# Optimization experiments

Measured on AMD Instinct MI355X. Metric: run time of the kernel, lower is better.

## Reference

```python
import jax, jax.numpy as jnp
import numpy as np

SEQ, B, IN_DIM, HID, OUT_DIM = 1024, 256, 131, 256, 131


def setup_inputs() -> dict:
    key = jax.random.key(0)
    ks = jax.random.split(key, 24)
    def p(k, shape):
        return (jax.random.normal(k, shape, dtype=jnp.float32) * 0.1)
    inp = {
        'X': jax.random.normal(ks[0], (SEQ, B, IN_DIM), dtype=jnp.float32),
        'Y': jax.random.normal(ks[1], (SEQ - 1, B, IN_DIM), dtype=jnp.float32),
        # encoder layer 0 (input -> hidden) and layer 1 (hidden -> hidden)
        'enc_Wih0': p(ks[2], (HID, IN_DIM)), 'enc_Whh0': p(ks[3], (HID, HID)),
        'enc_bih0': p(ks[4], (HID,)),        'enc_bhh0': p(ks[5], (HID,)),
        'enc_Wih1': p(ks[6], (HID, HID)),    'enc_Whh1': p(ks[7], (HID, HID)),
        'enc_bih1': p(ks[8], (HID,)),        'enc_bhh1': p(ks[9], (HID,)),
        # decoder RNNCells
        'dec_Wih0': p(ks[10], (HID, IN_DIM)), 'dec_Whh0': p(ks[11], (HID, HID)),
        'dec_bih0': p(ks[12], (HID,)),        'dec_bhh0': p(ks[13], (HID,)),
        'dec_Wih1': p(ks[14], (HID, HID)),    'dec_Whh1': p(ks[15], (HID, HID)),
        'dec_bih1': p(ks[16], (HID,)),        'dec_bhh1': p(ks[17], (HID,)),
        # output projection
        'lin_W': p(ks[18], (OUT_DIM, HID)), 'lin_b': p(ks[19], (OUT_DIM,)),
    }
    return inp


def _rnn_layer(seq, h0, Wih, Whh, bih, bhh):
    # Elman RNN layer: h_t = tanh(x_t Wih^T + bih + h_{t-1} Whh^T + bhh)
    def step(h, x):
        h = jnp.tanh(x @ Wih.T + bih + h @ Whh.T + bhh)
        return h, h
    hT, outs = jax.lax.scan(step, h0, seq)
    return outs, hT


def reference(X, Y,
              enc_Wih0, enc_Whh0, enc_bih0, enc_bhh0,
              enc_Wih1, enc_Whh1, enc_bih1, enc_bhh1,
              dec_Wih0, dec_Whh0, dec_bih0, dec_bhh0,
              dec_Wih1, dec_Whh1, dec_bih1, dec_bhh1,
              lin_W, lin_b):
    B_ = X.shape[1]
    H = enc_Whh0.shape[0]
    h0 = jnp.zeros((B_, H), X.dtype)
    # Encoder consumes X[:-1]
    out0, hn0 = _rnn_layer(X[:-1], h0, enc_Wih0, enc_Whh0, enc_bih0, enc_bhh0)
    out1, hn1 = _rnn_layer(out0, h0, enc_Wih1, enc_Whh1, enc_bih1, enc_bhh1)
    # Decoder (teacher forcing): inputs are X[-1], Y[0], ..., Y[T_out-2]
    T_out = X.shape[0] - 1
    dec_in = jnp.concatenate([X[-1:], Y[:T_out - 1]], axis=0)  # [T_out, B, in_dim]
    def dec_step(carry, x):
        h0c, h1c = carry
        h0n = jnp.tanh(x @ dec_Wih0.T + dec_bih0 + h0c @ dec_Whh0.T + dec_bhh0)
        h1n = jnp.tanh(h0n @ dec_Wih1.T + dec_bih1 + h1c @ dec_Whh1.T + dec_bhh1)
        logits = h1n @ lin_W.T + lin_b
        return (h0n, h1n), jax.nn.log_softmax(logits, axis=-1)
    _, Ypred = jax.lax.scan(dec_step, (hn0, hn1), dec_in)
    return Ypred  # [T_out, B, out_dim]
```

## Files before the change

### kernel.cpp

```cpp
#include <hip/hip_runtime.h>
#include <cstddef>


typedef __attribute__((ext_vector_type(8))) short short8;
typedef __attribute__((ext_vector_type(4))) float f32x4;

namespace {
constexpr int TSTEPS = 1023;
constexpr int BATCH = 256;
constexpr int IND = 131;
constexpr int OUTD = 131;
constexpr int MTOT = TSTEPS * BATCH;

constexpr size_t SB = (size_t)MTOT * 256 * 4;
constexpr int UE0 = 0;
constexpr int UE1 = 131072;
constexpr int UD0 = 262144;
constexpr int UD1 = 393216;
constexpr int EW0 = 524288;
constexpr int DW0 = 606208;
constexpr int EW1 = 688128;
constexpr int DW1 = 819200;
constexpr int LINP = 950272;
constexpr int PK_USH = 1024000;
constexpr size_t PKB = 2 * SB;
constexpr size_t BFB = PKB + 2 * (size_t)PK_USH;
constexpr int FIN0 = 1168;
constexpr int FIN1 = 1168 + 65536;
constexpr size_t TOTAL_WS = BFB + (size_t)(1168 + 2 * 65536) * 4;

constexpr int OFF_EW0s = 0, OFF_EH0s = 33792, OFF_EW1s = 99328, OFF_EH1s = 164864;
constexpr int OFF_DW0s = 230400, OFF_DH0s = 264192, OFF_DW1s = 329728, OFF_DH1s = 395264;
constexpr int OFF_LWs = 460800, OFF_EB0s = 494336, OFF_EB1s = 494592;
constexpr int OFF_DB0s = 494848, OFF_DB1s = 495104;
constexpr int WS_TOTAL_SLOW = 495360;
}

__device__ __forceinline__ unsigned short f2bf(float x) {
  unsigned u = __float_as_uint(x);
  u += 0x7fffu + ((u >> 16) & 1u);
  return (unsigned short)(u >> 16);
}
__device__ __forceinline__ float bf2f(unsigned short h) {
  return __uint_as_float(((unsigned)h) << 16);
}
__device__ __forceinline__ float ftanh(float x) {
  const float ax = fabsf(x);
  const float e = __expf(-2.f * ax);
  const float t = __fdividef(1.f - e, 1.f + e);
  return copysignf(t, x);
}
__device__ __forceinline__ f32x4 mfma16(uint4 a, uint4 b, f32x4 c) {
  return __builtin_amdgcn_mfma_f32_16x16x32_bf16(
      __builtin_bit_cast(short8, a), __builtin_bit_cast(short8, b), c, 0, 0, 0);
}

__global__ void prep_pack(
    const float* __restrict__ eW0, const float* __restrict__ eH0,
    const float* __restrict__ eb_ih0, const float* __restrict__ eb_hh0,
    const float* __restrict__ eW1, const float* __restrict__ eH1,
    const float* __restrict__ eb_ih1, const float* __restrict__ eb_hh1,
    const float* __restrict__ dW0, const float* __restrict__ dH0,
    const float* __restrict__ db_ih0, const float* __restrict__ db_hh0,
    const float* __restrict__ dW1, const float* __restrict__ dH1,
    const float* __restrict__ db_ih1, const float* __restrict__ db_hh1,
    const float* __restrict__ linW, const float* __restrict__ linb,
    unsigned short* __restrict__ pk, float* __restrict__ bfin) {
  const int e = blockIdx.x * 256 + threadIdx.x;
  if (e >= 513168) return;
  if (e < 262144) {
    const int um = e >> 16, le = e & 65535;
    const int j = le & 7, lane = (le >> 3) & 63, tile = (le >> 9) & 15, kk = le >> 13;
    const int n = tile * 16 + (lane & 15), k = kk * 32 + ((lane >> 4) << 3) + j;
    const float* U = (um == 0) ? eH0 : (um == 1) ? eH1 : (um == 2) ? dH0 : dH1;
    const float x = U[n * 256 + k];
    const unsigned short h = f2bf(x);
    const int base = um * 131072;
    pk[base + le] = h;
    pk[base + 65536 + le] = f2bf(x - bf2f(h));
  } else if (e < 344064) {
    const bool isD = (e >= 303104);
    const int e2 = e - (isD ? 303104 : 262144);
    const int j = e2 & 7, lane = (e2 >> 3) & 63, tile = (e2 >> 9) & 15, kk = e2 >> 13;
    const int n = tile * 16 + (lane & 15), k = kk * 32 + ((lane >> 4) << 3) + j;
    const float* W = isD ? dW0 : eW0;
    const float x = (k < IND) ? W[n * IND + k] : 0.f;
    const unsigned short h = f2bf(x);
    const int base = isD ? DW0 : EW0;
    pk[base + e2] = h;
    pk[base + 40960 + e2] = f2bf(x - bf2f(h));
  } else if (e < 475136) {
    const bool isD = (e >= 409600);
    const int e2 = e - (isD ? 409600 : 344064);
    const int j = e2 & 7, lane = (e2 >> 3) & 63, tile = (e2 >> 9) & 15, kk = e2 >> 13;
    const int n = tile * 16 + (lane & 15), k = kk * 32 + ((lane >> 4) << 3) + j;
    const float* W = isD ? dW1 : eW1;
    const float x = W[n * 256 + k];
    const unsigned short h = f2bf(x);
    const int base = isD ? DW1 : EW1;
    pk[base + e2] = h;
    pk[base + 65536 + e2] = f2bf(x - bf2f(h));
  } else if (e < 512000) {
    const int e2 = e - 475136;
    const int kk = e2 / 4608;
    const int rem = e2 - kk * 4608;
    const int t9 = rem >> 9, le = rem & 511;
    const int j = le & 7, lane = le >> 3;
    const int n = t9 * 16 + (lane & 15), k = kk * 32 + ((lane >> 4) << 3) + j;
    const float x = (n < OUTD) ? linW[n * 256 + k] : 0.f;
    const unsigned short h = f2bf(x);
    pk[LINP + e2] = h;
    pk[LINP + 36864 + e2] = f2bf(x - bf2f(h));
  } else {
    const int e3 = e - 512000;
    if (e3 < 256) bfin[e3] = eb_ih0[e3] + eb_hh0[e3];
    else if (e3 < 512) { const int j = e3 - 256; bfin[e3] = eb_ih1[j] + eb_hh1[j]; }
    else if (e3 < 768) { const int j = e3 - 512; bfin[e3] = db_ih0[j] + db_hh0[j]; }
    else if (e3 < 1024){ const int j = e3 - 768; bfin[e3] = db_ih1[j] + db_hh1[j]; }
    else { const int j = e3 - 1024; bfin[e3] = (j < OUTD) ? linb[j] : -1e30f; }
  }
}

__global__ __launch_bounds__(256) void gemm_proj(
    const float* __restrict__ A, const float* __restrict__ X1023,
    const float* __restrict__ Yp, const int amode, const int K, const int KK,
    const unsigned short* __restrict__ Wh, const unsigned short* __restrict__ Wl,
    const float* __restrict__ bias, float* __restrict__ Pout) {
  __shared__ unsigned short Ah[64][40];
  __shared__ unsigned short Al[64][40];
  const int tid = threadIdx.x, lane = tid & 63, wid = tid >> 6;
  const int mbase = blockIdx.x * 64;
  const int cg = blockIdx.y;
  const int srow = tid >> 2, kidx = (tid & 3) << 3;
  const float* rowptr;
  {
    const int grow = mbase + srow;
    if (amode) {
      const int t = grow >> 8, b = grow & 255;
      rowptr = t ? (Yp + ((size_t)(t - 1) * 256 + b) * IND) : (X1023 + (size_t)b * IND);
    } else {
      rowptr = A + (size_t)grow * K;
    }
  }
  const f32x4 z = {0.f, 0.f, 0.f, 0.f};
  f32x4 acc[4] = {z, z, z, z};
  const uint4* Wh4 = (const uint4*)Wh;
  const uint4* Wl4 = (const uint4*)Wl;
  for (int kk = 0; kk < KK; ++kk) {
    const int k0 = kk << 5;
    __syncthreads();
    float v[8];
#pragma unroll
    for (int j = 0; j < 8; ++j) {
      const int kg = k0 + kidx + j;
      v[j] = (kg < K) ? rowptr[kg] : 0.f;
    }
#pragma unroll
    for (int j = 0; j < 8; ++j) {
      const unsigned short h = f2bf(v[j]);
      Ah[srow][kidx + j] = h;
      Al[srow][kidx + j] = f2bf(v[j] - bf2f(h));
    }
    __syncthreads();
    const uint4 avh = *(const uint4*)&Ah[(wid << 4) + (lane & 15)][(lane >> 4) << 3];
    const uint4 avl = *(const uint4*)&Al[(wid << 4) + (lane & 15)][(lane >> 4) << 3];
#pragma unroll
    for (int tt = 0; tt < 4; ++tt) {
      const int bi = ((kk << 4) + (cg << 2) + tt) * 64 + lane;
      const uint4 bh = Wh4[bi], bl = Wl4[bi];
      acc[tt] = mfma16(avh, bh, acc[tt]);
      acc[tt] = mfma16(avh, bl, acc[tt]);
      acc[tt] = mfma16(avl, bh, acc[tt]);
    }
  }
#pragma unroll
  for (int tt = 0; tt < 4; ++tt) {
    const int col = ((cg << 2) + tt) * 16 + (lane & 15);
    const float bcol = bias[col];
#pragma unroll
    for (int r = 0; r < 4; ++r) {
      const int row = mbase + (wid << 4) + ((lane >> 4) << 2) + r;
      Pout[(size_t)row * 256 + col] = acc[tt][r] + bcol;
    }
  }
}

__global__ __launch_bounds__(512, 2) void scan_kernel(
    const float* __restrict__ Pin, float* __restrict__ Pout,
    const unsigned short* __restrict__ Uh,
    const float* __restrict__ hinit, float* __restrict__ finals) {
  __shared__ unsigned short Ah[2][16][264];
  __shared__ unsigned short Al[2][16][264];
  const int tid = threadIdx.x, lane = tid & 63, wid = tid >> 6;
  const int r0 = blockIdx.x << 4;
  const uint4* U4 = (const uint4*)Uh;
  uint4 uf[2][2][8];
#pragma unroll
  for (int tt = 0; tt < 2; ++tt)
#pragma unroll
    for (int kk = 0; kk < 8; ++kk) {
      const int idx = ((kk << 4) + wid * 2 + tt) * 64 + lane;
      uf[0][tt][kk] = U4[idx];
      uf[1][tt][kk] = U4[idx + 8192];
    }
#pragma unroll
  for (int j = 0; j < 8; ++j) {
    const int e = tid * 8 + j;
    const int row = e >> 8, col = e & 255;
    const float x = hinit ? hinit[((r0 + row) << 8) + col] : 0.f;
    const unsigned short h = f2bf(x);
    Ah[0][row][col] = h;
    Al[0][row][col] = f2bf(x - bf2f(h));
  }
  __syncthreads();
  const int rowl = (lane >> 4) << 2;
  const int col0 = (wid * 2) * 16 + (lane & 15);
  const float* pin_base = Pin + (((size_t)(r0 + rowl)) << 8) + col0;
  float* pout_base = Pout ? (Pout + (((size_t)(r0 + rowl)) << 8) + col0) : (float*)0;
  float* fbase = finals ? (finals + (((size_t)(r0 + rowl)) << 8) + col0) : (float*)0;
  float pc[2][4];
#pragma unroll
  for (int tt = 0; tt < 2; ++tt)
#pragma unroll
    for (int r = 0; r < 4; ++r) pc[tt][r] = pin_base[tt * 16 + r * 256];
  for (int t = 0; t < TSTEPS; ++t) {
    const int cur = t & 1, nxt = cur ^ 1;
    float pn[2][4];
    {
      const int tn = (t + 1 < TSTEPS) ? (t + 1) : t;
      const float* ptn = pin_base + (size_t)tn * 65536;
#pragma unroll
      for (int tt = 0; tt < 2; ++tt)
#pragma unroll
        for (int r = 0; r < 4; ++r) pn[tt][r] = ptn[tt * 16 + r * 256];
    }
    const f32x4 z = {0.f, 0.f, 0.f, 0.f};
    f32x4 hh[2] = {z, z}, hl[2] = {z, z}, lh[2] = {z, z};
#pragma unroll
    for (int kk = 0; kk < 8; ++kk) {
      const uint4 avh = *(const uint4*)&Ah[cur][lane & 15][(kk << 5) + ((lane >> 4) << 3)];
      const uint4 avl = *(const uint4*)&Al[cur][lane & 15][(kk << 5) + ((lane >> 4) << 3)];
      hh[0] = mfma16(avh, uf[0][0][kk], hh[0]);
      hh[1] = mfma16(avh, uf[0][1][kk], hh[1]);
      hl[0] = mfma16(avh, uf[1][0][kk], hl[0]);
      hl[1] = mfma16(avh, uf[1][1][kk], hl[1]);
      lh[0] = mfma16(avl, uf[0][0][kk], lh[0]);
      lh[1] = mfma16(avl, uf[0][1][kk], lh[1]);
    }
    float* pot = pout_base ? (pout_base + (size_t)t * 65536) : (float*)0;
#pragma unroll
    for (int tt = 0; tt < 2; ++tt) {
#pragma unroll
      for (int r = 0; r < 4; ++r) {
        const float av = (hh[tt][r] + hl[tt][r]) + lh[tt][r];
        const float x = ftanh(av + pc[tt][r]);
        if (pot) pot[tt * 16 + r * 256] = x;
        if (fbase && t == TSTEPS - 1) fbase[tt * 16 + r * 256] = x;
        const unsigned short h = f2bf(x);
        Ah[nxt][rowl + r][col0 + tt * 16] = h;
        Al[nxt][rowl + r][col0 + tt * 16] = f2bf(x - bf2f(h));
      }
    }
    asm volatile("s_waitcnt lgkmcnt(0)\n\ts_barrier" ::: "memory");
#pragma unroll
    for (int tt = 0; tt < 2; ++tt)
#pragma unroll
      for (int r = 0; r < 4; ++r) pc[tt][r] = pn[tt][r];
  }
}

__global__ __launch_bounds__(256) void head_kernel(
    const float* __restrict__ A, const unsigned short* __restrict__ Wh,
    const unsigned short* __restrict__ Wl, const float* __restrict__ biasp,
    float* __restrict__ out) {
  __shared__ unsigned short Ah[64][40];
  __shared__ unsigned short Al[64][40];
  const int tid = threadIdx.x, lane = tid & 63, wid = tid >> 6;
  const int mbase = blockIdx.x * 64;
  const int srow = tid >> 2, kidx = (tid & 3) << 3;
  const float* rowptr = A + (size_t)(mbase + srow) * 256;
  const f32x4 z = {0.f, 0.f, 0.f, 0.f};
  f32x4 acc[9] = {z, z, z, z, z, z, z, z, z};
  const uint4* Wh4 = (const uint4*)Wh;
  const uint4* Wl4 = (const uint4*)Wl;
  for (int kk = 0; kk < 8; ++kk) {
    const int k0 = kk << 5;
    __syncthreads();
#pragma unroll
    for (int j = 0; j < 8; ++j) {
      const float v = rowptr[k0 + kidx + j];
      const unsigned short h = f2bf(v);
      Ah[srow][kidx + j] = h;
      Al[srow][kidx + j] = f2bf(v - bf2f(h));
    }
    __syncthreads();
    const uint4 avh = *(const uint4*)&Ah[(wid << 4) + (lane & 15)][(lane >> 4) << 3];
    const uint4 avl = *(const uint4*)&Al[(wid << 4) + (lane & 15)][(lane >> 4) << 3];
#pragma unroll
    for (int tt = 0; tt < 9; ++tt) {
      const int bi = (kk * 9 + tt) * 64 + lane;
      const uint4 bh = Wh4[bi], bl = Wl4[bi];
      acc[tt] = mfma16(avh, bh, acc[tt]);
      acc[tt] = mfma16(avh, bl, acc[tt]);
      acc[tt] = mfma16(avl, bh, acc[tt]);
    }
  }
#pragma unroll
  for (int tt = 0; tt < 9; ++tt) {
    const float b = biasp[tt * 16 + (lane & 15)];
#pragma unroll
    for (int r = 0; r < 4; ++r) acc[tt][r] += b;
  }
  float lse[4];
#pragma unroll
  for (int r = 0; r < 4; ++r) {
    float m = acc[0][r];
#pragma unroll
    for (int tt = 1; tt < 9; ++tt) m = fmaxf(m, acc[tt][r]);
    m = fmaxf(m, __shfl_xor(m, 1));
    m = fmaxf(m, __shfl_xor(m, 2));
    m = fmaxf(m, __shfl_xor(m, 4));
    m = fmaxf(m, __shfl_xor(m, 8));
    float s = 0.f;
#pragma unroll
    for (int tt = 0; tt < 9; ++tt) s += __expf(acc[tt][r] - m);
    s += __shfl_xor(s, 1);
    s += __shfl_xor(s, 2);
    s += __shfl_xor(s, 4);
    s += __shfl_xor(s, 8);
    lse[r] = m + __logf(s);
  }
#pragma unroll
  for (int tt = 0; tt < 9; ++tt) {
    const int col = tt * 16 + (lane & 15);
    if (col < OUTD) {
#pragma unroll
      for (int r = 0; r < 4; ++r) {
        const int row = mbase + (wid << 4) + ((lane >> 4) << 2) + r;
        out[(size_t)row * OUTD + col] = acc[tt][r] - lse[r];
      }
    }
  }
}

__device__ __forceinline__ void packWs(float* __restrict__ ws, const float* __restrict__ src,
                                       int e, int off, int K, int ncols) {
  const int le = e - off;
  const int m = le & 3;
  const int tt = le >> 2;
  const int j = tt % ncols;
// ... 122 lines not shown
    __syncthreads();
    h1s[0][tid] = n1a; h1s[1][tid] = n1b;
    __syncthreads();
  }
  for (int t = 0; t < TSTEPS; ++t) {
    const float* xbase = (t == 0) ? (X + (size_t)TSTEPS * BATCH * IND)
                                  : (Y + (size_t)(t - 1) * BATCH * IND);
    {
      const int r = tid / 132, i = tid - r * 132;
      xb[r][i] = (i < IND) ? xbase[(size_t)(r0 + r) * IND + i] : 0.f;
      if (tid < 8) {
        const int i2 = tid + 124;
        xb[1][i2] = (i2 < IND) ? xbase[(size_t)(r0 + 1) * IND + i2] : 0.f;
      }
    }
    __syncthreads();
    const float2 a = layer_in(dw0, dh0, xb[0], xb[1], h0s[0], h0s[1], db0v, tid);
    const float n0a = ftanh(a.x), n0b = ftanh(a.y);
    __syncthreads();
    h0s[0][tid] = n0a; h0s[1][tid] = n0b;
    __syncthreads();
    const float2 b = layer_hh(dw1, dh1, h0s[0], h0s[1], h1s[0], h1s[1], db1v, tid);
    const float n1a = ftanh(b.x), n1b = ftanh(b.y);
    __syncthreads();
    h1s[0][tid] = n1a; h1s[1][tid] = n1b;
    __syncthreads();
    if (tid < OUTD) {
      float c0 = linb[tid], c1 = linb[tid];
#pragma unroll 4
      for (int k4 = 0; k4 < 64; ++k4) {
        const float4 w = lw[k4 * OUTD + tid];
        c0 = dot4(*(const float4*)&h1s[0][k4 * 4], w, c0);
        c1 = dot4(*(const float4*)&h1s[1][k4 * 4], w, c1);
      }
      lo[0][tid] = c0;
      lo[1][tid] = c1;
    }
    __syncthreads();
    const int wid = tid >> 6, lane = tid & 63;
    if (wid < 2) {
      float m = -3.0e38f;
      for (int o = lane; o < OUTD; o += 64) m = fmaxf(m, lo[wid][o]);
#pragma unroll
      for (int off = 32; off > 0; off >>= 1) m = fmaxf(m, __shfl_xor(m, off, 64));
      float s = 0.f;
      for (int o = lane; o < OUTD; o += 64) s += __expf(lo[wid][o] - m);
#pragma unroll
      for (int off = 32; off > 0; off >>= 1) s += __shfl_xor(s, off, 64);
      const float lse = m + __logf(s);
      float* op = out + ((size_t)t * BATCH + r0 + wid) * OUTD;
      for (int o = lane; o < OUTD; o += 64) op[o] = lo[wid][o] - lse;
    }
    __syncthreads();
  }
}

extern "C" void kernel_launch(void* const* d_in, const int* in_sizes, int n_in,
                              void* d_out, int out_size, void* d_ws, size_t ws_size,
                              hipStream_t stream) {
  const float* X      = (const float*)d_in[0];
  const float* Y      = (const float*)d_in[1];
  const float* eW0    = (const float*)d_in[2];
  const float* eH0    = (const float*)d_in[3];
  const float* eb_ih0 = (const float*)d_in[4];
  const float* eb_hh0 = (const float*)d_in[5];
  const float* eW1    = (const float*)d_in[6];
  const float* eH1    = (const float*)d_in[7];
  const float* eb_ih1 = (const float*)d_in[8];
  const float* eb_hh1 = (const float*)d_in[9];
  const float* dW0    = (const float*)d_in[10];
  const float* dH0    = (const float*)d_in[11];
  const float* db_ih0 = (const float*)d_in[12];
  const float* db_hh0 = (const float*)d_in[13];
  const float* dW1    = (const float*)d_in[14];
  const float* dH1    = (const float*)d_in[15];
  const float* db_ih1 = (const float*)d_in[16];
  const float* db_hh1 = (const float*)d_in[17];
  const float* linW   = (const float*)d_in[18];
  const float* linb   = (const float*)d_in[19];
  float* out = (float*)d_out;

  if (ws_size >= TOTAL_WS) {
    float* buf0 = (float*)d_ws;
    float* buf1 = (float*)((char*)d_ws + SB);
    unsigned short* pk = (unsigned short*)((char*)d_ws + PKB);
    float* bfin = (float*)((char*)d_ws + BFB);
    float* be0 = bfin, *be1 = bfin + 256, *bd0 = bfin + 512, *bd1 = bfin + 768;
    float* blin = bfin + 1024;
    float* fin0 = bfin + FIN0;
    float* fin1 = bfin + FIN1;
    const float* X1023 = X + (size_t)TSTEPS * BATCH * IND;

    prep_pack<<<2005, 256, 0, stream>>>(eW0, eH0, eb_ih0, eb_hh0, eW1, eH1, eb_ih1,
                                        eb_hh1, dW0, dH0, db_ih0, db_hh0, dW1, dH1,
                                        db_ih1, db_hh1, linW, linb, pk, bfin);
    gemm_proj<<<dim3(MTOT / 64, 4), 256, 0, stream>>>(
        X, nullptr, nullptr, 0, IND, 5, pk + EW0, pk + EW0 + 40960, be0, buf0);
    scan_kernel<<<16, 512, 0, stream>>>(buf0, buf1, pk + UE0, nullptr, fin0);
    gemm_proj<<<dim3(MTOT / 64, 4), 256, 0, stream>>>(
        buf1, nullptr, nullptr, 0, 256, 8, pk + EW1, pk + EW1 + 65536, be1, buf0);
    scan_kernel<<<16, 512, 0, stream>>>(buf0, nullptr, pk + UE1, nullptr, fin1);
    gemm_proj<<<dim3(MTOT / 64, 4), 256, 0, stream>>>(
        nullptr, X1023, Y, 1, IND, 5, pk + DW0, pk + DW0 + 40960, bd0, buf1);
    scan_kernel<<<16, 512, 0, stream>>>(buf1, buf0, pk + UD0, fin0, nullptr);
    gemm_proj<<<dim3(MTOT / 64, 4), 256, 0, stream>>>(
        buf0, nullptr, nullptr, 0, 256, 8, pk + DW1, pk + DW1 + 65536, bd1, buf1);
    scan_kernel<<<16, 512, 0, stream>>>(buf1, buf0, pk + UD1, fin1, nullptr);
    head_kernel<<<MTOT / 64, 256, 0, stream>>>(buf0, pk + LINP, pk + LINP + 36864,
                                               blin, out);
  } else {
    float* ws = (float*)d_ws;
    prep_slow<<<(WS_TOTAL_SLOW + 255) / 256, 256, 0, stream>>>(
        eW0, eH0, eb_ih0, eb_hh0, eW1, eH1, eb_ih1, eb_hh1,
        dW0, dH0, db_ih0, db_hh0, dW1, dH1, db_ih1, db_hh1, linW, ws);
    rnn_slow<<<128, 256, 0, stream>>>(X, Y, ws, linb, out);
  }
}
```

Before: 9.209 ms.

## Halve scan block to 4 waves with 4 column tiles and interleaved hi/lo LDS

The recurrent scan kernel now runs 256 threads (4 waves) per block instead of 512. Each wave covers 64 output columns (4 MFMA tiles) and keeps twice as many Whh fragments in registers. The split-bf16 hidden state is stored as packed hi/lo 32-bit words in one LDS array and unpacked with perm instructions. The aim is cheaper per-step barriers and more MFMA work per wave, at the cost of higher register pressure and fewer waves to hide latency on the serial dependency chain.

After: 11.95 ms. 29.7% more time.

```diff
diff --git a/kernel.cpp b/kernel.cpp
--- a/kernel.cpp
+++ b/kernel.cpp
@@ -43,6 +43,11 @@
 }
 __device__ __forceinline__ float bf2f(unsigned short h) {
   return __uint_as_float(((unsigned)h) << 16);
+}
+__device__ __forceinline__ unsigned packbf(float x) {
+  const unsigned short h = f2bf(x);
+  const unsigned short l = f2bf(x - bf2f(h));
+  return ((unsigned)l << 16) | (unsigned)h;
 }
 __device__ __forceinline__ float ftanh(float x) {
   const float ax = fabsf(x);
@@ -185,85 +190,90 @@
   }
 }
 
-__global__ __launch_bounds__(512, 2) void scan_kernel(
+__global__ __launch_bounds__(256, 1) void scan_kernel(
     const float* __restrict__ Pin, float* __restrict__ Pout,
     const unsigned short* __restrict__ Uh,
     const float* __restrict__ hinit, float* __restrict__ finals) {
-  __shared__ unsigned short Ah[2][16][264];
-  __shared__ unsigned short Al[2][16][264];
+  __shared__ unsigned A2[2][16][260];
   const int tid = threadIdx.x, lane = tid & 63, wid = tid >> 6;
   const int r0 = blockIdx.x << 4;
   const uint4* U4 = (const uint4*)Uh;
-  uint4 uf[2][2][8];
-#pragma unroll
-  for (int tt = 0; tt < 2; ++tt)
+  uint4 uf[2][4][8];
+#pragma unroll
+  for (int tt = 0; tt < 4; ++tt)
 #pragma unroll
     for (int kk = 0; kk < 8; ++kk) {
-      const int idx = ((kk << 4) + wid * 2 + tt) * 64 + lane;
+      const int idx = ((kk << 4) + (wid << 2) + tt) * 64 + lane;
       uf[0][tt][kk] = U4[idx];
       uf[1][tt][kk] = U4[idx + 8192];
     }
 #pragma unroll
-  for (int j = 0; j < 8; ++j) {
-    const int e = tid * 8 + j;
+  for (int j = 0; j < 16; ++j) {
+    const int e = tid * 16 + j;
     const int row = e >> 8, col = e & 255;
     const float x = hinit ? hinit[((r0 + row) << 8) + col] : 0.f;
-    const unsigned short h = f2bf(x);
-    Ah[0][row][col] = h;
-    Al[0][row][col] = f2bf(x - bf2f(h));
+    A2[0][row][col] = packbf(x);
   }
   __syncthreads();
   const int rowl = (lane >> 4) << 2;
-  const int col0 = (wid * 2) * 16 + (lane & 15);
-  const float* pin_base = Pin + (((size_t)(r0 + rowl)) << 8) + col0;
-  float* pout_base = Pout ? (Pout + (((size_t)(r0 + rowl)) << 8) + col0) : (float*)0;
-  float* fbase = finals ? (finals + (((size_t)(r0 + rowl)) << 8) + col0) : (float*)0;
-  float pc[2][4];
-#pragma unroll
-  for (int tt = 0; tt < 2; ++tt)
+  const int colb = (wid << 6) + (lane & 15);
+  const float* pin_base = Pin + (((size_t)(r0 + rowl)) << 8) + colb;
+  float* pout_base = Pout ? (Pout + (((size_t)(r0 + rowl)) << 8) + colb) : (float*)0;
+  float* fbase = finals ? (finals + (((size_t)(r0 + rowl)) << 8) + colb) : (float*)0;
+  float pc[4][4];
+#pragma unroll
+  for (int tt = 0; tt < 4; ++tt)
 #pragma unroll
     for (int r = 0; r < 4; ++r) pc[tt][r] = pin_base[tt * 16 + r * 256];
   for (int t = 0; t < TSTEPS; ++t) {
     const int cur = t & 1, nxt = cur ^ 1;
-    float pn[2][4];
+    float pn[4][4];
     {
       const int tn = (t + 1 < TSTEPS) ? (t + 1) : t;
       const float* ptn = pin_base + (size_t)tn * 65536;
 #pragma unroll
-      for (int tt = 0; tt < 2; ++tt)
+      for (int tt = 0; tt < 4; ++tt)
 #pragma unroll
         for (int r = 0; r < 4; ++r) pn[tt][r] = ptn[tt * 16 + r * 256];
     }
     const f32x4 z = {0.f, 0.f, 0.f, 0.f};
-    f32x4 hh[2] = {z, z}, hl[2] = {z, z}, lh[2] = {z, z};
+    f32x4 hh[4] = {z, z, z, z}, hl[4] = {z, z, z, z}, lh[4] = {z, z, z, z};
 #pragma unroll
     for (int kk = 0; kk < 8; ++kk) {
-      const uint4 avh = *(const uint4*)&Ah[cur][lane & 15][(kk << 5) + ((lane >> 4) << 3)];
-      const uint4 avl = *(const uint4*)&Al[cur][lane & 15][(kk << 5) + ((lane >> 4) << 3)];
-      hh[0] = mfma16(avh, uf[0][0][kk], hh[0]);
-      hh[1] = mfma16(avh, uf[0][1][kk], hh[1]);
-      hl[0] = mfma16(avh, uf[1][0][kk], hl[0]);
-      hl[1] = mfma16(avh, uf[1][1][kk], hl[1]);
-      lh[0] = mfma16(avl, uf[0][0][kk], lh[0]);
-      lh[1] = mfma16(avl, uf[0][1][kk], lh[1]);
+      const int koff = (kk << 5) + ((lane >> 4) << 3);
+      const uint4 p0 = *(const uint4*)&A2[cur][lane & 15][koff];
+      const uint4 p1 = *(const uint4*)&A2[cur][lane & 15][koff + 4];
+      uint4 avh, avl;
+      avh.x = __builtin_amdgcn_perm(p0.y, p0.x, 0x05040100u);
+      avh.y = __builtin_amdgcn_perm(p0.w, p0.z, 0x05040100u);
+      avh.z = __builtin_amdgcn_perm(p1.y, p1.x, 0x05040100u);
+      avh.w = __builtin_amdgcn_perm(p1.w, p1.z, 0x05040100u);
+      avl.x = __builtin_amdgcn_perm(p0.y, p0.x, 0x07060302u);
+      avl.y = __builtin_amdgcn_perm(p0.w, p0.z, 0x07060302u);
+      avl.z = __builtin_amdgcn_perm(p1.y, p1.x, 0x07060302u);
+      avl.w = __builtin_amdgcn_perm(p1.w, p1.z, 0x07060302u);
+#pragma unroll
+      for (int tt = 0; tt < 4; ++tt) {
+        hh[tt] = mfma16(avh, uf[0][tt][kk], hh[tt]);
+        hl[tt] = mfma16(avh, uf[1][tt][kk], hl[tt]);
+        lh[tt] = mfma16(avl, uf[0][tt][kk], lh[tt]);
+      }
     }
     float* pot = pout_base ? (pout_base + (size_t)t * 65536) : (float*)0;
 #pragma unroll
-    for (int tt = 0; tt < 2; ++tt) {
+    for (int tt = 0; tt < 4; ++tt) {
 #pragma unroll
       for (int r = 0; r < 4; ++r) {
         const float av = (hh[tt][r] + hl[tt][r]) + lh[tt][r];
         const float x = ftanh(av + pc[tt][r]);
         if (pot) pot[tt * 16 + r * 256] = x;
         if (fbase && t == TSTEPS - 1) fbase[tt * 16 + r * 256] = x;
-        const unsigned short h = f2bf(x);
-        Ah[nxt][rowl + r][col0 + tt * 16] = h;
-        Al[nxt][rowl + r][col0 + tt * 16] = f2bf(x - bf2f(h));
+        A2[nxt][rowl + r][colb + tt * 16] = packbf(x);
       }
     }
     asm volatile("s_waitcnt lgkmcnt(0)\n\ts_barrier" ::: "memory");
 #pragma unroll
-    for (int tt = 0; tt < 2; ++tt)
+    for (int tt = 0; tt < 4; ++tt)
 #pragma unroll
       for (int r = 0; r < 4; ++r) pc[tt][r] = pn[tt][r];
   }
@@ -568,16 +578,16 @@
                                         db_ih1, db_hh1, linW, linb, pk, bfin);
     gemm_proj<<<dim3(MTOT / 64, 4), 256, 0, stream>>>(
         X, nullptr, nullptr, 0, IND, 5, pk + EW0, pk + EW0 + 40960, be0, buf0);
-    scan_kernel<<<16, 512, 0, stream>>>(buf0, buf1, pk + UE0, nullptr, fin0);
+    scan_kernel<<<16, 256, 0, stream>>>(buf0, buf1, pk + UE0, nullptr, fin0);
     gemm_proj<<<dim3(MTOT / 64, 4), 256, 0, stream>>>(
         buf1, nullptr, nullptr, 0, 256, 8, pk + EW1, pk + EW1 + 65536, be1, buf0);
-    scan_kernel<<<16, 512, 0, stream>>>(buf0, nullptr, pk + UE1, nullptr, fin1);
+    scan_kernel<<<16, 256, 0, stream>>>(buf0, nullptr, pk + UE1, nullptr, fin1);
     gemm_proj<<<dim3(MTOT / 64, 4), 256, 0, stream>>>(
         nullptr, X1023, Y, 1, IND, 5, pk + DW0, pk + DW0 + 40960, bd0, buf1);
-    scan_kernel<<<16, 512, 0, stream>>>(buf1, buf0, pk + UD0, fin0, nullptr);
+    scan_kernel<<<16, 256, 0, stream>>>(buf1, buf0, pk + UD0, fin0, nullptr);
     gemm_proj<<<dim3(MTOT / 64, 4), 256, 0, stream>>>(
         buf0, nullptr, nullptr, 0, 256, 8, pk + DW1, pk + DW1 + 65536, bd1, buf1);
-    scan_kernel<<<16, 512, 0, stream>>>(buf1, buf0, pk + UD1, fin1, nullptr);
+    scan_kernel<<<16, 256, 0, stream>>>(buf1, buf0, pk + UD1, fin1, nullptr);
     head_kernel<<<MTOT / 64, 256, 0, stream>>>(buf0, pk + LINP, pk + LINP + 36864,
                                                blin, out);
   } else {
```

## Fuse stacked RNN layers into a pipelined producer/consumer kernel with ring buffers

Applied to the files above, without the earlier changes.

Replaces the four sequential per-layer scan kernels and the two intermediate layer-1 input GEMMs with two pipe kernels, one for the encoder and one for the decoder. In each pipe kernel, separate block groups run the layer-0 recurrence, the layer-1 input projection and the layer-1 recurrence concurrently. Data moves between them through global ring buffers holding bf16 hi/lo pairs, and atomic flags track progress. The hidden state is also packed as hi/lo bf16 in one 32-bit word and unpacked with perm instructions. The aim is to overlap the two layers' serial time loops and drop full-sequence intermediate traffic. The cost is cross-block spin-waiting, reliance on all blocks being co-resident, and bounded polling (POLLCAP) that could read stale data if a producer falls far behind.

Result: slower. 22.53 ms (+144.7%).

```diff
diff --git a/kernel.cpp b/kernel.cpp
--- a/kernel.cpp
+++ b/kernel.cpp
@@ -11,6 +11,8 @@
 constexpr int IND = 131;
 constexpr int OUTD = 131;
 constexpr int MTOT = TSTEPS * BATCH;
+constexpr int RING = 256;
+constexpr int POLLCAP = 8192;
 
 constexpr size_t SB = (size_t)MTOT * 256 * 4;
 constexpr int UE0 = 0;
@@ -44,6 +46,11 @@
 __device__ __forceinline__ float bf2f(unsigned short h) {
   return __uint_as_float(((unsigned)h) << 16);
 }
+__device__ __forceinline__ unsigned packbf(float x) {
+  const unsigned short h = f2bf(x);
+  const unsigned short l = f2bf(x - bf2f(h));
+  return ((unsigned)l << 16) | (unsigned)h;
+}
 __device__ __forceinline__ float ftanh(float x) {
   const float ax = fabsf(x);
   const float e = __expf(-2.f * ax);
@@ -53,6 +60,17 @@
 __device__ __forceinline__ f32x4 mfma16(uint4 a, uint4 b, f32x4 c) {
   return __builtin_amdgcn_mfma_f32_16x16x32_bf16(
       __builtin_bit_cast(short8, a), __builtin_bit_cast(short8, b), c, 0, 0, 0);
+}
+__device__ __forceinline__ void unpack_pair(uint4 p0, uint4 p1,
+                                            uint4& avh, uint4& avl) {
+  avh.x = __builtin_amdgcn_perm(p0.y, p0.x, 0x05040100u);
+  avh.y = __builtin_amdgcn_perm(p0.w, p0.z, 0x05040100u);
+  avh.z = __builtin_amdgcn_perm(p1.y, p1.x, 0x05040100u);
+  avh.w = __builtin_amdgcn_perm(p1.w, p1.z, 0x05040100u);
+  avl.x = __builtin_amdgcn_perm(p0.y, p0.x, 0x07060302u);
+  avl.y = __builtin_amdgcn_perm(p0.w, p0.z, 0x07060302u);
+  avl.z = __builtin_amdgcn_perm(p1.y, p1.x, 0x07060302u);
+  avl.w = __builtin_amdgcn_perm(p1.w, p1.z, 0x07060302u);
 }
 
 __global__ void prep_pack(
@@ -65,9 +83,11 @@
     const float* __restrict__ dW1, const float* __restrict__ dH1,
     const float* __restrict__ db_ih1, const float* __restrict__ db_hh1,
     const float* __restrict__ linW, const float* __restrict__ linb,
-    unsigned short* __restrict__ pk, float* __restrict__ bfin) {
+    unsigned short* __restrict__ pk, float* __restrict__ bfin,
+    int* __restrict__ cnt0) {
   const int e = blockIdx.x * 256 + threadIdx.x;
-  if (e >= 513168) return;
+  if (e >= 513680) return;
+  if (e >= 513168) { cnt0[e - 513168] = 0; return; }
   if (e < 262144) {
     const int um = e >> 16, le = e & 65535;
     const int j = le & 7, lane = (le >> 3) & 63, tile = (le >> 9) & 15, kk = le >> 13;
@@ -185,15 +205,112 @@
   }
 }
 
-__global__ __launch_bounds__(512, 2) void scan_kernel(
-    const float* __restrict__ Pin, float* __restrict__ Pout,
-    const unsigned short* __restrict__ Uh,
-    const float* __restrict__ hinit, float* __restrict__ finals) {
-  __shared__ unsigned short Ah[2][16][264];
-  __shared__ unsigned short Al[2][16][264];
+__global__ __launch_bounds__(512, 2) void pipe_kernel(
+    const float* __restrict__ Pin,
+    unsigned* __restrict__ xring,
+    unsigned* __restrict__ p1ring,
+    int* __restrict__ cnt,
+    const unsigned short* __restrict__ U0p,
+    const unsigned short* __restrict__ W1p,
+    const float* __restrict__ b1,
+    const unsigned short* __restrict__ U1p,
+    const float* __restrict__ h0init, const float* __restrict__ h1init,
+    float* __restrict__ fin0out, float* __restrict__ fin1out,
+    float* __restrict__ outBuf) {
+  __shared__ __align__(16) unsigned A2[2][16][260];
   const int tid = threadIdx.x, lane = tid & 63, wid = tid >> 6;
-  const int r0 = blockIdx.x << 4;
-  const uint4* U4 = (const uint4*)Uh;
+  const int bid = blockIdx.x;
+  const int role = bid >> 4;
+  const int g = bid & 15;
+  const int r0g = g << 4;
+  const int rowl = (lane >> 4) << 2;
+  const int colb = (wid << 5) + (lane & 15);
+  const f32x4 z = {0.f, 0.f, 0.f, 0.f};
+
+  if (role == 1) {
+    const uint4* W4 = (const uint4*)W1p;
+    uint4 wf[2][2][8];
+#pragma unroll
+    for (int tt = 0; tt < 2; ++tt)
+#pragma unroll
+      for (int kk = 0; kk < 8; ++kk) {
+        const int idx = ((kk << 4) + wid * 2 + tt) * 64 + lane;
+        wf[0][tt][kk] = W4[idx];
+        wf[1][tt][kk] = W4[idx + 8192];
+      }
+    const float btt0 = b1[colb], btt1 = b1[colb + 16];
+    const unsigned* xr_g = xring + (size_t)g * RING * 4096;
+    unsigned* pr_g = p1ring + (size_t)g * RING * 8 * 512;
+    int* flagX = cnt + g;
+    int* myflag = cnt + 32 + g * 8 + wid;
+    int* cons1p = cnt + 160 + g;
+    int cachedProd = 0, cachedCons = 0;
+    for (int t = 0; t < TSTEPS; ++t) {
+      if (cachedProd <= t) {
+        int nv = 0;
+        if (lane == 0) {
+          int v = cachedProd, it = 0;
+          while (v <= t && ++it < POLLCAP) v = atomicAdd(flagX, 0);
+          nv = v;
+        }
+        cachedProd = __shfl(nv, 0);
+        __threadfence();
+      }
+      if (t - cachedCons >= RING - 64) {
+        int nv = 0;
+        if (lane == 0) {
+          int v = cachedCons, it = 0;
+          while (t - v >= RING - 64 && ++it < POLLCAP) v = atomicAdd(cons1p, 0);
+          nv = v;
+        }
+        cachedCons = __shfl(nv, 0);
+      }
+      const unsigned* xt = xr_g + (size_t)(t & (RING - 1)) * 4096;
+      f32x4 hh[2] = {z, z}, hl[2] = {z, z}, lh[2] = {z, z};
+#pragma unroll
+      for (int kk = 0; kk < 8; ++kk) {
+        const unsigned* base = xt + (lane & 15) * 256 + (kk << 5) + ((lane >> 4) << 3);
+        const uint4 p0 = *(const uint4*)base;
+        const uint4 p1v = *(const uint4*)(base + 4);
+        uint4 avh, avl;
+        unpack_pair(p0, p1v, avh, avl);
+        hh[0] = mfma16(avh, wf[0][0][kk], hh[0]);
+        hh[1] = mfma16(avh, wf[0][1][kk], hh[1]);
+        hl[0] = mfma16(avh, wf[1][0][kk], hl[0]);
+        hl[1] = mfma16(avh, wf[1][1][kk], hl[1]);
+        lh[0] = mfma16(avl, wf[0][0][kk], lh[0]);
+        lh[1] = mfma16(avl, wf[0][1][kk], lh[1]);
+      }
+      uint4 oa, ob;
+      {
+        unsigned o[8];
+#pragma unroll
+        for (int tt = 0; tt < 2; ++tt) {
+          const float bb = tt ? btt1 : btt0;
+#pragma unroll
+          for (int r = 0; r < 4; ++r) {
+            const float pv = (hh[tt][r] + hl[tt][r]) + lh[tt][r] + bb;
+            o[tt * 4 + r] = packbf(pv);
+          }
+        }
+        oa = make_uint4(o[0], o[1], o[2], o[3]);
+        ob = make_uint4(o[4], o[5], o[6], o[7]);
+      }
+      unsigned* dst = pr_g + ((size_t)(t & (RING - 1)) * 8 + wid) * 512 + lane * 8;
+      *(uint4*)dst = oa;
+      *(uint4*)(dst + 4) = ob;
+      __threadfence();
+      if (lane == 0) atomicExch(myflag, t + 1);
+      if ((t & 31) == 31) {
+        __syncthreads();
+        if (tid == 0) atomicExch(cnt + 16 + g, t + 1);
+      }
+    }
+    return;
+  }
+
+  const unsigned short* Up = (role == 0) ? U0p : U1p;
+  const uint4* U4 = (const uint4*)Up;
   uint4 uf[2][2][8];
 #pragma unroll
   for (int tt = 0; tt < 2; ++tt)
@@ -203,69 +320,144 @@
       uf[0][tt][kk] = U4[idx];
       uf[1][tt][kk] = U4[idx + 8192];
     }
-#pragma unroll
-  for (int j = 0; j < 8; ++j) {
-    const int e = tid * 8 + j;
-    const int row = e >> 8, col = e & 255;
-    const float x = hinit ? hinit[((r0 + row) << 8) + col] : 0.f;
-    const unsigned short h = f2bf(x);
-    Ah[0][row][col] = h;
-    Al[0][row][col] = f2bf(x - bf2f(h));
+  {
+    const float* hinit = (role == 0) ? h0init : h1init;
+#pragma unroll
+    for (int j = 0; j < 8; ++j) {
+      const int e = tid * 8 + j;
+      const int row = e >> 8, col = e & 255;
+      const float x = hinit ? hinit[((r0g + row) << 8) + col] : 0.f;
+      A2[0][row][col] = packbf(x);
+    }
   }
   __syncthreads();
-  const int rowl = (lane >> 4) << 2;
-  const int col0 = (wid * 2) * 16 + (lane & 15);
-  const float* pin_base = Pin + (((size_t)(r0 + rowl)) << 8) + col0;
-  float* pout_base = Pout ? (Pout + (((size_t)(r0 + rowl)) << 8) + col0) : (float*)0;
-  float* fbase = finals ? (finals + (((size_t)(r0 + rowl)) << 8) + col0) : (float*)0;
-  float pc[2][4];
-#pragma unroll
-  for (int tt = 0; tt < 2; ++tt)
-#pragma unroll
-    for (int r = 0; r < 4; ++r) pc[tt][r] = pin_base[tt * 16 + r * 256];
-  for (int t = 0; t < TSTEPS; ++t) {
-    const int cur = t & 1, nxt = cur ^ 1;
-    float pn[2][4];
-    {
-      const int tn = (t + 1 < TSTEPS) ? (t + 1) : t;
-      const float* ptn = pin_base + (size_t)tn * 65536;
+  float* fbase;
+  {
+    float* ft = (role == 0) ? fin0out : fin1out;
+    fbase = ft ? (ft + ((size_t)(r0g + rowl) << 8) + colb) : (float*)0;
+  }
+
+  if (role == 0) {
+    const float* pin_base = Pin + ((size_t)(r0g + rowl) << 8) + colb;
+    unsigned* xr_g = xring + (size_t)g * RING * 4096;
+    int* flag = cnt + g;
+    int* consp = cnt + 16 + g;
+    int cachedCons = 0;
+    float pc[2][4];
+#pragma unroll
+    for (int tt = 0; tt < 2; ++tt)
+#pragma unroll
+      for (int r = 0; r < 4; ++r) pc[tt][r] = pin_base[tt * 16 + r * 256];
+    for (int t = 0; t < TSTEPS; ++t) {
+      const int cur = t & 1, nxt = cur ^ 1;
+      if (t - cachedCons >= RING - 64) {
+        int nv = 0;
+        if (lane == 0) {
+          int v = cachedCons, it = 0;
+          while (t - v >= RING - 64 && ++it < POLLCAP) v = atomicAdd(consp, 0);
+          nv = v;
+        }
+        cachedCons = __shfl(nv, 0);
+      }
+      float pn[2][4];
+      {
+        const int tn = (t + 1 < TSTEPS) ? (t + 1) : t;
+        const float* ptn = pin_base + (size_t)tn * 65536;
+#pragma unroll
+        for (int tt = 0; tt < 2; ++tt)
+#pragma unroll
+          for (int r = 0; r < 4; ++r) pn[tt][r] = ptn[tt * 16 + r * 256];
+      }
+      f32x4 hh[2] = {z, z}, hl[2] = {z, z}, lh[2] = {z, z};
+#pragma unroll
+      for (int kk = 0; kk < 8; ++kk) {
+        const int koff = (kk << 5) + ((lane >> 4) << 3);
+        const uint4 p0 = *(const uint4*)&A2[cur][lane & 15][koff];
+        const uint4 p1v = *(const uint4*)&A2[cur][lane & 15][koff + 4];
+        uint4 avh, avl;
+        unpack_pair(p0, p1v, avh, avl);
+        hh[0] = mfma16(avh, uf[0][0][kk], hh[0]);
+        hh[1] = mfma16(avh, uf[0][1][kk], hh[1]);
+        hl[0] = mfma16(avh, uf[1][0][kk], hl[0]);
+        hl[1] = mfma16(avh, uf[1][1][kk], hl[1]);
+        lh[0] = mfma16(avl, uf[0][0][kk], lh[0]);
+        lh[1] = mfma16(avl, uf[0][1][kk], lh[1]);
+      }
+      unsigned* xt = xr_g + (size_t)(t & (RING - 1)) * 4096;
+#pragma unroll
+      for (int tt = 0; tt < 2; ++tt) {
+#pragma unroll
+        for (int r = 0; r < 4; ++r) {
+          const float av = (hh[tt][r] + hl[tt][r]) + lh[tt][r];
+          const float x = ftanh(av + pc[tt][r]);
+          const unsigned u = packbf(x);
+          A2[nxt][rowl + r][colb + tt * 16] = u;
+          xt[(rowl + r) * 256 + colb + tt * 16] = u;
+          if (fbase && t == TSTEPS - 1) fbase[tt * 16 + r * 256] = x;
+        }
+      }
+      __threadfence();
+      __syncthreads();
+      if (tid == 0) atomicExch(flag, t + 1);
 #pragma unroll
       for (int tt = 0; tt < 2; ++tt)
 #pragma unroll
-        for (int r = 0; r < 4; ++r) pn[tt][r] = ptn[tt * 16 + r * 256];
-    }
-    const f32x4 z = {0.f, 0.f, 0.f, 0.f};
-    f32x4 hh[2] = {z, z}, hl[2] = {z, z}, lh[2] = {z, z};
-#pragma unroll
-    for (int kk = 0; kk < 8; ++kk) {
-      const uint4 avh = *(const uint4*)&Ah[cur][lane & 15][(kk << 5) + ((lane >> 4) << 3)];
-      const uint4 avl = *(const uint4*)&Al[cur][lane & 15][(kk << 5) + ((lane >> 4) << 3)];
-      hh[0] = mfma16(avh, uf[0][0][kk], hh[0]);
-      hh[1] = mfma16(avh, uf[0][1][kk], hh[1]);
-      hl[0] = mfma16(avh, uf[1][0][kk], hl[0]);
-      hl[1] = mfma16(avh, uf[1][1][kk], hl[1]);
-      lh[0] = mfma16(avl, uf[0][0][kk], lh[0]);
-      lh[1] = mfma16(avl, uf[0][1][kk], lh[1]);
-    }
-    float* pot = pout_base ? (pout_base + (size_t)t * 65536) : (float*)0;
-#pragma unroll
-    for (int tt = 0; tt < 2; ++tt) {
-#pragma unroll
-      for (int r = 0; r < 4; ++r) {
-        const float av = (hh[tt][r] + hl[tt][r]) + lh[tt][r];
-        const float x = ftanh(av + pc[tt][r]);
-        if (pot) pot[tt * 16 + r * 256] = x;
-        if (fbase && t == TSTEPS - 1) fbase[tt * 16 + r * 256] = x;
-        const unsigned short h = f2bf(x);
-        Ah[nxt][rowl + r][col0 + tt * 16] = h;
-        Al[nxt][rowl + r][col0 + tt * 16] = f2bf(x - bf2f(h));
-      }
-    }
-    asm volatile("s_waitcnt lgkmcnt(0)\n\ts_barrier" ::: "memory");
-#pragma unroll
-    for (int tt = 0; tt < 2; ++tt)
-#pragma unroll
-      for (int r = 0; r < 4; ++r) pc[tt][r] = pn[tt][r];
+        for (int r = 0; r < 4; ++r) pc[tt][r] = pn[tt][r];
+    }
+  } else {
+    const unsigned* pr_g = p1ring + (size_t)g * RING * 8 * 512;
+    int* myflag = cnt + 32 + g * 8 + wid;
+    float* outb = outBuf ? (outBuf + ((size_t)(r0g + rowl) << 8) + colb) : (float*)0;
+    int cachedProd = 0;
+    for (int t = 0; t < TSTEPS; ++t) {
+      const int cur = t & 1, nxt = cur ^ 1;
+      if (cachedProd <= t) {
+        int nv = 0;
+        if (lane == 0) {
+          int v = cachedProd, it = 0;
+          while (v <= t && ++it < POLLCAP) v = atomicAdd(myflag, 0);
+          nv = v;
+        }
+        cachedProd = __shfl(nv, 0);
+        __threadfence();
+      }
+      const unsigned* src = pr_g + ((size_t)(t & (RING - 1)) * 8 + wid) * 512 + lane * 8;
+      const uint4 pa = *(const uint4*)src;
+      const uint4 pb = *(const uint4*)(src + 4);
+      f32x4 hh[2] = {z, z}, hl[2] = {z, z}, lh[2] = {z, z};
+#pragma unroll
+      for (int kk = 0; kk < 8; ++kk) {
+        const int koff = (kk << 5) + ((lane >> 4) << 3);
+        const uint4 p0 = *(const uint4*)&A2[cur][lane & 15][koff];
+        const uint4 p1v = *(const uint4*)&A2[cur][lane & 15][koff + 4];
+        uint4 avh, avl;
+        unpack_pair(p0, p1v, avh, avl);
+        hh[0] = mfma16(avh, uf[0][0][kk], hh[0]);
+        hh[1] = mfma16(avh, uf[0][1][kk], hh[1]);
+        hl[0] = mfma16(avh, uf[1][0][kk], hl[0]);
+        hl[1] = mfma16(avh, uf[1][1][kk], hl[1]);
+        lh[0] = mfma16(avl, uf[0][0][kk], lh[0]);
+        lh[1] = mfma16(avl, uf[0][1][kk], lh[1]);
+      }
+      float* pot = outb ? (outb + (size_t)t * 65536) : (float*)0;
+#pragma unroll
+      for (int tt = 0; tt < 2; ++tt) {
+#pragma unroll
+        for (int r = 0; r < 4; ++r) {
+          const unsigned pu = tt ? ((r == 0) ? pb.x : (r == 1) ? pb.y : (r == 2) ? pb.z : pb.w)
+                                 : ((r == 0) ? pa.x : (r == 1) ? pa.y : (r == 2) ? pa.z : pa.w);
+          const float p = bf2f((unsigned short)(pu & 0xffffu)) +
+                          bf2f((unsigned short)(pu >> 16));
+          const float av = (hh[tt][r] + hl[tt][r]) + lh[tt][r];
+          const float x = ftanh(av + p);
+          A2[nxt][rowl + r][colb + tt * 16] = packbf(x);
+          if (pot) pot[tt * 16 + r * 256] = x;
+          if (fbase && t == TSTEPS - 1) fbase[tt * 16 + r * 256] = x;
+        }
+      }
+      asm volatile("s_waitcnt lgkmcnt(0)\n\ts_barrier" ::: "memory");
+      if ((t & 31) == 31 && tid == 0) atomicExch(cnt + 160 + g, t + 1);
+    }
   }
 }
 
@@ -554,7 +746,11 @@
 
   if (ws_size >= TOTAL_WS) {
     float* buf0 = (float*)d_ws;
-    float* buf1 = (float*)((char*)d_ws + SB);
+    unsigned* ring = (unsigned*)((char*)d_ws + SB);
+    unsigned* xring = ring;
+    unsigned* p1ring = ring + (size_t)16 * RING * 4096;
+    int* cnt_e = (int*)((char*)d_ws + 2 * SB - 4096);
+    int* cnt_d = cnt_e + 256;
     unsigned short* pk = (unsigned short*)((char*)d_ws + PKB);
     float* bfin = (float*)((char*)d_ws + BFB);
     float* be0 = bfin, *be1 = bfin + 256, *bd0 = bfin + 512, *bd1 = bfin + 768;
@@ -563,21 +759,19 @@
     float* fin1 = bfin + FIN1;
     const float* X1023 = X + (size_t)TSTEPS * BATCH * IND;
 
-    prep_pack<<<2005, 256, 0, stream>>>(eW0, eH0, eb_ih0, eb_hh0, eW1, eH1, eb_ih1,
+    prep_pack<<<2007, 256, 0, stream>>>(eW0, eH0, eb_ih0, eb_hh0, eW1, eH1, eb_ih1,
                                         eb_hh1, dW0, dH0, db_ih0, db_hh0, dW1, dH1,
-                                        db_ih1, db_hh1, linW, linb, pk, bfin);
+                                        db_ih1, db_hh1, linW, linb, pk, bfin, cnt_e);
     gemm_proj<<<dim3(MTOT / 64, 4), 256, 0, stream>>>(
         X, nullptr, nullptr, 0, IND, 5, pk + EW0, pk + EW0 + 40960, be0, buf0);
-    scan_kernel<<<16, 512, 0, stream>>>(buf0, buf1, pk + UE0, nullptr, fin0);
+    pipe_kernel<<<48, 512, 0, stream>>>(
+        buf0, xring, p1ring, cnt_e, pk + UE0, pk + EW1, be1, pk + UE1,
+        nullptr, nullptr, fin0, fin1, nullptr);
     gemm_proj<<<dim3(MTOT / 64, 4), 256, 0, stream>>>(
-        buf1, nullptr, nullptr, 0, 256, 8, pk + EW1, pk + EW1 + 65536, be1, buf0);
-    scan_kernel<<<16, 512, 0, stream>>>(buf0, nullptr, pk + UE1, nullptr, fin1);
-    gemm_proj<<<dim3(MTOT / 64, 4), 256, 0, stream>>>(
-        nullptr, X1023, Y, 1, IND, 5, pk + DW0, pk + DW0 + 40960, bd0, buf1);
-    scan_kernel<<<16, 512, 0, stream>>>(buf1, buf0, pk + UD0, fin0, nullptr);
-    gemm_proj<<<dim3(MTOT / 64, 4), 256, 0, stream>>>(
-        buf0, nullptr, nullptr, 0, 256, 8, pk + DW1, pk + DW1 + 65536, bd1, buf1);
-    scan_kernel<<<16, 512, 0, stream>>>(buf1, buf0, pk + UD1, fin1, nullptr);
+        nullptr, X1023, Y, 1, IND, 5, pk + DW0, pk + DW0 + 40960, bd0, buf0);
+    pipe_kernel<<<48, 512, 0, stream>>>(
+        buf0, xring, p1ring, cnt_d, pk + UD0, pk + DW1, bd1, pk + UD1,
+        fin0, fin1, nullptr, nullptr, buf0);
     head_kernel<<<MTOT / 64, 256, 0, stream>>>(buf0, pk + LINP, pk + LINP + 36864,
                                                blin, out);
   } else {
```

## Run encoder layer-1 and decoder layer-0 scans concurrently; pack hi/lo bf16 in LDS

Applied to the files above, without the earlier changes.

The encoder layer-1 recurrence and the decoder layer-0 recurrence do not depend on each other. A new scan2_kernel runs both in one 32-block launch, so only three sequential latency-bound scans remain instead of four, and the launch order and buffers are rearranged to allow this. Scans now write their outputs in place over their input projections. The hidden-state hi/lo bf16 split is stored as one packed 32-bit LDS word and unpacked with perm instructions, which halves the LDS stores per step but adds ALU unpack work. The in-place writes alias pointers that are declared restrict, which is a correctness risk.

After: 8.135 ms. -11.7%, faster.

```diff
diff --git a/kernel.cpp b/kernel.cpp
--- a/kernel.cpp
+++ b/kernel.cpp
@@ -44,6 +44,11 @@
 __device__ __forceinline__ float bf2f(unsigned short h) {
   return __uint_as_float(((unsigned)h) << 16);
 }
+__device__ __forceinline__ unsigned packbf(float x) {
+  const unsigned short h = f2bf(x);
+  const unsigned short l = f2bf(x - bf2f(h));
+  return ((unsigned)l << 16) | (unsigned)h;
+}
 __device__ __forceinline__ float ftanh(float x) {
   const float ax = fabsf(x);
   const float e = __expf(-2.f * ax);
@@ -53,6 +58,17 @@
 __device__ __forceinline__ f32x4 mfma16(uint4 a, uint4 b, f32x4 c) {
   return __builtin_amdgcn_mfma_f32_16x16x32_bf16(
       __builtin_bit_cast(short8, a), __builtin_bit_cast(short8, b), c, 0, 0, 0);
+}
+__device__ __forceinline__ void unpack_pair(uint4 p0, uint4 p1,
+                                            uint4& avh, uint4& avl) {
+  avh.x = __builtin_amdgcn_perm(p0.y, p0.x, 0x05040100u);
+  avh.y = __builtin_amdgcn_perm(p0.w, p0.z, 0x05040100u);
+  avh.z = __builtin_amdgcn_perm(p1.y, p1.x, 0x05040100u);
+  avh.w = __builtin_amdgcn_perm(p1.w, p1.z, 0x05040100u);
+  avl.x = __builtin_amdgcn_perm(p0.y, p0.x, 0x07060302u);
+  avl.y = __builtin_amdgcn_perm(p0.w, p0.z, 0x07060302u);
+  avl.z = __builtin_amdgcn_perm(p1.y, p1.x, 0x07060302u);
+  avl.w = __builtin_amdgcn_perm(p1.w, p1.z, 0x07060302u);
 }
 
 __global__ void prep_pack(
@@ -185,14 +201,13 @@
   }
 }
 
-__global__ __launch_bounds__(512, 2) void scan_kernel(
+__device__ __forceinline__ void scan_body(
     const float* __restrict__ Pin, float* __restrict__ Pout,
     const unsigned short* __restrict__ Uh,
-    const float* __restrict__ hinit, float* __restrict__ finals) {
-  __shared__ unsigned short Ah[2][16][264];
-  __shared__ unsigned short Al[2][16][264];
+    const float* __restrict__ hinit, float* __restrict__ finals,
+    const int r0) {
+  __shared__ __align__(16) unsigned A2[2][16][260];
   const int tid = threadIdx.x, lane = tid & 63, wid = tid >> 6;
-  const int r0 = blockIdx.x << 4;
   const uint4* U4 = (const uint4*)Uh;
   uint4 uf[2][2][8];
 #pragma unroll
@@ -208,16 +223,15 @@
     const int e = tid * 8 + j;
     const int row = e >> 8, col = e & 255;
     const float x = hinit ? hinit[((r0 + row) << 8) + col] : 0.f;
-    const unsigned short h = f2bf(x);
-    Ah[0][row][col] = h;
-    Al[0][row][col] = f2bf(x - bf2f(h));
+    A2[0][row][col] = packbf(x);
   }
   __syncthreads();
   const int rowl = (lane >> 4) << 2;
-  const int col0 = (wid * 2) * 16 + (lane & 15);
+  const int col0 = wid * 32 + (lane & 15);
   const float* pin_base = Pin + (((size_t)(r0 + rowl)) << 8) + col0;
   float* pout_base = Pout ? (Pout + (((size_t)(r0 + rowl)) << 8) + col0) : (float*)0;
   float* fbase = finals ? (finals + (((size_t)(r0 + rowl)) << 8) + col0) : (float*)0;
+  const f32x4 z = {0.f, 0.f, 0.f, 0.f};
   float pc[2][4];
 #pragma unroll
   for (int tt = 0; tt < 2; ++tt)
@@ -234,12 +248,14 @@
 #pragma unroll
         for (int r = 0; r < 4; ++r) pn[tt][r] = ptn[tt * 16 + r * 256];
     }
-    const f32x4 z = {0.f, 0.f, 0.f, 0.f};
     f32x4 hh[2] = {z, z}, hl[2] = {z, z}, lh[2] = {z, z};
 #pragma unroll
     for (int kk = 0; kk < 8; ++kk) {
-      const uint4 avh = *(const uint4*)&Ah[cur][lane & 15][(kk << 5) + ((lane >> 4) << 3)];
-      const uint4 avl = *(const uint4*)&Al[cur][lane & 15][(kk << 5) + ((lane >> 4) << 3)];
+      const int koff = (kk << 5) + ((lane >> 4) << 3);
+      const uint4 p0 = *(const uint4*)&A2[cur][lane & 15][koff];
+      const uint4 p1v = *(const uint4*)&A2[cur][lane & 15][koff + 4];
+      uint4 avh, avl;
+      unpack_pair(p0, p1v, avh, avl);
       hh[0] = mfma16(avh, uf[0][0][kk], hh[0]);
       hh[1] = mfma16(avh, uf[0][1][kk], hh[1]);
       hl[0] = mfma16(avh, uf[1][0][kk], hl[0]);
@@ -256,9 +272,7 @@
         const float x = ftanh(av + pc[tt][r]);
         if (pot) pot[tt * 16 + r * 256] = x;
         if (fbase && t == TSTEPS - 1) fbase[tt * 16 + r * 256] = x;
-        const unsigned short h = f2bf(x);
-        Ah[nxt][rowl + r][col0 + tt * 16] = h;
-        Al[nxt][rowl + r][col0 + tt * 16] = f2bf(x - bf2f(h));
+        A2[nxt][rowl + r][col0 + tt * 16] = packbf(x);
       }
     }
     asm volatile("s_waitcnt lgkmcnt(0)\n\ts_barrier" ::: "memory");
@@ -266,6 +280,28 @@
     for (int tt = 0; tt < 2; ++tt)
 #pragma unroll
       for (int r = 0; r < 4; ++r) pc[tt][r] = pn[tt][r];
+  }
+}
+
+__global__ __launch_bounds__(512, 2) void scan_kernel(
+    const float* __restrict__ Pin, float* __restrict__ Pout,
+    const unsigned short* __restrict__ Uh,
+    const float* __restrict__ hinit, float* __restrict__ finals) {
+  scan_body(Pin, Pout, Uh, hinit, finals, blockIdx.x << 4);
+}
+
+__global__ __launch_bounds__(512, 2) void scan2_kernel(
+    const float* __restrict__ PinA, float* __restrict__ PoutA,
+    const unsigned short* __restrict__ UhA,
+    const float* __restrict__ hinitA, float* __restrict__ finalsA,
+    const float* __restrict__ PinB, float* __restrict__ PoutB,
+    const unsigned short* __restrict__ UhB,
+    const float* __restrict__ hinitB, float* __restrict__ finalsB) {
+  const int bid = blockIdx.x;
+  if (bid < 16) {
+    scan_body(PinA, PoutA, UhA, hinitA, finalsA, bid << 4);
+  } else {
+    scan_body(PinB, PoutB, UhB, hinitB, finalsB, (bid - 16) << 4);
   }
 }
 
@@ -568,17 +604,18 @@
                                         db_ih1, db_hh1, linW, linb, pk, bfin);
     gemm_proj<<<dim3(MTOT / 64, 4), 256, 0, stream>>>(
         X, nullptr, nullptr, 0, IND, 5, pk + EW0, pk + EW0 + 40960, be0, buf0);
-    scan_kernel<<<16, 512, 0, stream>>>(buf0, buf1, pk + UE0, nullptr, fin0);
+    scan_kernel<<<16, 512, 0, stream>>>(buf0, buf0, pk + UE0, nullptr, fin0);
     gemm_proj<<<dim3(MTOT / 64, 4), 256, 0, stream>>>(
-        buf1, nullptr, nullptr, 0, 256, 8, pk + EW1, pk + EW1 + 65536, be1, buf0);
-    scan_kernel<<<16, 512, 0, stream>>>(buf0, nullptr, pk + UE1, nullptr, fin1);
+        buf0, nullptr, nullptr, 0, 256, 8, pk + EW1, pk + EW1 + 65536, be1, buf1);
     gemm_proj<<<dim3(MTOT / 64, 4), 256, 0, stream>>>(
-        nullptr, X1023, Y, 1, IND, 5, pk + DW0, pk + DW0 + 40960, bd0, buf1);
-    scan_kernel<<<16, 512, 0, stream>>>(buf1, buf0, pk + UD0, fin0, nullptr);
+        nullptr, X1023, Y, 1, IND, 5, pk + DW0, pk + DW0 + 40960, bd0, buf0);
+    scan2_kernel<<<32, 512, 0, stream>>>(
+        buf1, nullptr, pk + UE1, nullptr, fin1,
+        buf0, buf0,   pk + UD0, fin0,   nullptr);
     gemm_proj<<<dim3(MTOT / 64, 4), 256, 0, stream>>>(
         buf0, nullptr, nullptr, 0, 256, 8, pk + DW1, pk + DW1 + 65536, bd1, buf1);
-    scan_kernel<<<16, 512, 0, stream>>>(buf1, buf0, pk + UD1, fin1, nullptr);
-    head_kernel<<<MTOT / 64, 256, 0, stream>>>(buf0, pk + LINP, pk + LINP + 36864,
+    scan_kernel<<<16, 512, 0, stream>>>(buf1, buf1, pk + UD1, fin1, nullptr);
+    head_kernel<<<MTOT / 64, 256, 0, stream>>>(buf1, pk + LINP, pk + LINP + 36864,
                                                blin, out);
   } else {
     float* ws = (float*)d_ws;
```
